# Kernel optimization log

Hardware: AMD Instinct MI355X
Metric: run time of the kernel (lower is better)

The kernel has to match this reference:

```python
import jax, jax.numpy as jnp
import numpy as np

N, E, G, F = 50000, 800000, 128, 64  # nodes, edges, graphs, feature dim
EPS = 1e-5


def setup_inputs() -> dict:
    key = jax.random.key(0)
    ks = jax.random.split(key, 16)
    w = lambda k, s: jax.random.normal(k, s, jnp.float32) * 0.05
    inp = {
        "x": jax.random.normal(ks[0], (N, F), jnp.float32),
        # SAGEConv l: lin_l (aggregated neighbors, with bias), lin_r (root, no bias)
        "c0_Wl": w(ks[1], (F, F)), "c0_bl": jnp.zeros((F,), jnp.float32), "c0_Wr": w(ks[2], (F, F)),
        "c1_Wl": w(ks[3], (F, F)), "c1_bl": jnp.zeros((F,), jnp.float32), "c1_Wr": w(ks[4], (F, F)),
        "c2_Wl": w(ks[5], (F, F)), "c2_bl": jnp.zeros((F,), jnp.float32), "c2_Wr": w(ks[6], (F, F)),
        # skip linears (bias=False)
        "s0_W": w(ks[7], (F, F)), "s1_W": w(ks[8], (F, F)),
        # graph-mode LayerNorm affine params
        "ln0_w": jnp.ones((F,), jnp.float32), "ln0_b": jnp.zeros((F,), jnp.float32),
        "ln1_w": jnp.ones((F,), jnp.float32), "ln1_b": jnp.zeros((F,), jnp.float32),
        "ln2_w": jnp.ones((F,), jnp.float32), "ln2_b": jnp.zeros((F,), jnp.float32),
        # PReLU(1): single shared slope, torch default init 0.25
        "p0_a": jnp.full((1,), 0.25, jnp.float32),
        "p1_a": jnp.full((1,), 0.25, jnp.float32),
        "p2_a": jnp.full((1,), 0.25, jnp.float32),
        "edge_index": jax.random.randint(ks[9], (2, E), 0, N, jnp.int64),
        "batch": jnp.sort(jax.random.randint(ks[10], (N,), 0, G, jnp.int64)),
    }
    return inp


def _sage(x, Wl, bl, Wr, src, dst):
    # mean-aggregate source features at destinations, then two linears
    agg = jax.ops.segment_sum(x[src], dst, num_segments=N)            # [N, F]
    deg = jax.ops.segment_sum(jnp.ones((E,), x.dtype), dst, num_segments=N)
    agg = agg / jnp.maximum(deg, 1.0)[:, None]
    return agg @ Wl + bl + x @ Wr


def _graph_ln(x, batch, w, b):
    # PyG LayerNorm mode='graph': normalize over all nodes & channels per graph
    f = x.shape[-1]
    cnt = jax.ops.segment_sum(jnp.ones((x.shape[0],), x.dtype), batch, num_segments=G)
    norm = jnp.maximum(cnt, 1.0) * f                                  # [G]
    mean = jax.ops.segment_sum(x, batch, num_segments=G).sum(-1) / norm
    xc = x - mean[batch][:, None]
    var = jax.ops.segment_sum(xc * xc, batch, num_segments=G).sum(-1) / norm
    out = xc / jnp.sqrt(var + EPS)[batch][:, None]
    return out * w + b


def _prelu(x, a):
    return jnp.where(x >= 0, x, a[0] * x)


def reference(x, c0_Wl, c0_bl, c0_Wr, c1_Wl, c1_bl, c1_Wr, c2_Wl, c2_bl, c2_Wr,
              s0_W, s1_W, ln0_w, ln0_b, ln1_w, ln1_b, ln2_w, ln2_b,
              p0_a, p1_a, p2_a, edge_index, batch):
    src, dst = edge_index[0], edge_index[1]
    h1 = _prelu(_graph_ln(_sage(x, c0_Wl, c0_bl, c0_Wr, src, dst), batch, ln0_w, ln0_b), p0_a)
    h2 = _sage(h1 + x @ s0_W, c1_Wl, c1_bl, c1_Wr, src, dst)
    h2 = _prelu(_graph_ln(h2, batch, ln1_w, ln1_b), p1_a)
    ret = _sage(h1 + h2 + x @ s1_W, c2_Wl, c2_bl, c2_Wr, src, dst)
    ret = _prelu(_graph_ln(ret, batch, ln2_w, ln2_b), p2_a)
    return ret
```

## Files before the change

kernel.cpp:

```cpp
#include <hip/hip_runtime.h>

#define NN 50000
#define NE 800000
#define NG 128
#define NF 64
#define EPSV 1e-5f
#define GB3 782
#define NBUCK 196
#define BCAP 5120

typedef unsigned short ushortT;

__device__ inline unsigned short f2bf(float f) {
  unsigned u = __float_as_uint(f);
  u += 0x7FFF + ((u >> 16) & 1);
  return (unsigned short)(u >> 16);
}

__global__ void k_bz(const int* __restrict__ batch, int* __restrict__ bound,
                     int* __restrict__ gcursor, float* __restrict__ stats) {
  int i = blockIdx.x * 256 + threadIdx.x;
  if (blockIdx.x == 0) {
    int t = threadIdx.x;
    if (t < NBUCK) gcursor[t] = 0;
    for (int k = t; k < 6 * NG; k += 256) stats[k] = 0.f;
  }
  if (i >= NN) return;
  int b1 = batch[i];
  int b0 = (i == 0) ? -1 : batch[i - 1];
  for (int g = b0 + 1; g <= b1; ++g) bound[g] = i;
  if (i == NN - 1) {
    for (int g = b1 + 1; g <= NG; ++g) bound[g] = NN;
  }
}

__global__ __launch_bounds__(256) void k_cvt(const float* __restrict__ in,
                                             ushortT* __restrict__ outb) {
  int t = blockIdx.x * 256 + threadIdx.x;
  if (t >= NN * NF / 4) return;
  float4 v = ((const float4*)in)[t];
  ushortT4_t: ;
  ushort4 o;
  o.x = f2bf(v.x); o.y = f2bf(v.y); o.z = f2bf(v.z); o.w = f2bf(v.w);
  ((ushort4*)outb)[t] = o;
}

__global__ __launch_bounds__(256) void k_binA(const int* __restrict__ src,
                                              const int* __restrict__ dst,
                                              int* __restrict__ gcursor,
                                              int2* __restrict__ bbuf) {
  __shared__ int cnt[NBUCK], base[NBUCK], rank[NBUCK];
  int tid = threadIdx.x;
  if (tid < NBUCK) { cnt[tid] = 0; rank[tid] = 0; }
  __syncthreads();
  int e0 = blockIdx.x * 4096;
  int sv[16], dv[16], bk[16];
#pragma unroll
  for (int i = 0; i < 16; ++i) {
    int e = e0 + i * 256 + tid;
    if (e < NE) {
      sv[i] = src[e];
      dv[i] = dst[e];
      bk[i] = dv[i] >> 8;
      atomicAdd(&cnt[bk[i]], 1);
    } else bk[i] = -1;
  }
  __syncthreads();
  if (tid < NBUCK && cnt[tid] > 0) base[tid] = atomicAdd(&gcursor[tid], cnt[tid]);
  __syncthreads();
#pragma unroll
  for (int i = 0; i < 16; ++i) {
    if (bk[i] >= 0) {
      int p = base[bk[i]] + atomicAdd(&rank[bk[i]], 1);
      if (p < BCAP) bbuf[(size_t)bk[i] * BCAP + p] = make_int2(sv[i], dv[i]);
    }
  }
}

__global__ __launch_bounds__(256) void k_bscan(const int* __restrict__ gcursor,
                                               int* __restrict__ bbase,
                                               int* __restrict__ off) {
  __shared__ int sh[256];
  int tid = threadIdx.x;
  int v = (tid < NBUCK) ? gcursor[tid] : 0;
  sh[tid] = v;
  __syncthreads();
  for (int d = 1; d < 256; d <<= 1) {
    int t = (tid >= d) ? sh[tid - d] : 0;
    __syncthreads();
    sh[tid] += t;
    __syncthreads();
  }
  if (tid < NBUCK) bbase[tid] = sh[tid] - v;
  if (tid == NBUCK - 1) { bbase[NBUCK] = sh[tid]; off[NN] = sh[tid]; }
}

__global__ __launch_bounds__(256) void k_binB(const int2* __restrict__ bbuf,
                                              const int* __restrict__ gcursor,
                                              const int* __restrict__ bbase,
                                              int* __restrict__ off,
                                              int* __restrict__ csr) {
  __shared__ int cnt[256], cur[256], sh[256];
  int tid = threadIdx.x;
  int b = blockIdx.x;
  int nb = gcursor[b]; if (nb > BCAP) nb = BCAP;
  int gbase = bbase[b];
  cnt[tid] = 0;
  __syncthreads();
  const int2* bp = bbuf + (size_t)b * BCAP;
  for (int i = tid; i < nb; i += 256) {
    atomicAdd(&cnt[bp[i].y & 255], 1);
  }
  __syncthreads();
  int v = cnt[tid];
  sh[tid] = v;
  __syncthreads();
  for (int d = 1; d < 256; d <<= 1) {
    int t = (tid >= d) ? sh[tid - d] : 0;
    __syncthreads();
    sh[tid] += t;
    __syncthreads();
  }
  int excl = sh[tid] - v;
  cur[tid] = excl;
  int node = b * 256 + tid;
  if (node < NN) off[node] = gbase + excl;
  __syncthreads();
  for (int i = tid; i < nb; i += 256) {
    int2 e = bp[i];
    int p = atomicAdd(&cur[e.y & 255], 1);
    csr[gbase + p] = e.x;
  }
}

__global__ __launch_bounds__(256) void k_agg(const ushortT* __restrict__ in,
                                             const int* __restrict__ off,
                                             const int* __restrict__ csr,
                                             float* __restrict__ out) {
  int t = blockIdx.x * 256 + threadIdx.x;
  int node = t >> 6;
  int lane = threadIdx.x & 63;
  int eo = lane >> 3;
  int fl = (lane & 7) << 3;
  if (node >= NN) return;
  int s0 = off[node], s1 = off[node + 1];
  float a0 = 0.f, a1 = 0.f, a2 = 0.f, a3 = 0.f, a4 = 0.f, a5 = 0.f, a6 = 0.f, a7 = 0.f;
  for (int j = s0 + eo; j < s1; j += 8) {
    int s = csr[j];
    uint4 v = *(const uint4*)&in[(size_t)s * NF + fl];
    a0 += __uint_as_float(v.x << 16);
    a1 += __uint_as_float(v.x & 0xFFFF0000u);
    a2 += __uint_as_float(v.y << 16);
    a3 += __uint_as_float(v.y & 0xFFFF0000u);
    a4 += __uint_as_float(v.z << 16);
    a5 += __uint_as_float(v.z & 0xFFFF0000u);
    a6 += __uint_as_float(v.w << 16);
    a7 += __uint_as_float(v.w & 0xFFFF0000u);
  }
#pragma unroll
  for (int d = 8; d < 64; d <<= 1) {
    a0 += __shfl_xor(a0, d); a1 += __shfl_xor(a1, d);
    a2 += __shfl_xor(a2, d); a3 += __shfl_xor(a3, d);
    a4 += __shfl_xor(a4, d); a5 += __shfl_xor(a5, d);
    a6 += __shfl_xor(a6, d); a7 += __shfl_xor(a7, d);
  }
  if (eo == 0) {
    int dg = s1 - s0;
    float inv = (dg > 0) ? 1.f / (float)dg : 0.f;
    float4* op = (float4*)&out[(size_t)node * NF + fl];
    op[0] = make_float4(a0 * inv, a1 * inv, a2 * inv, a3 * inv);
    op[1] = make_float4(a4 * inv, a5 * inv, a6 * inv, a7 * inv);
  }
}

__global__ __launch_bounds__(256) void k_sage_linear(const float* __restrict__ A,
                                                     const float* __restrict__ X,
                                                     const float* __restrict__ Wl,
                                                     const float* __restrict__ bl,
                                                     const float* __restrict__ Wr,
                                                     const int* __restrict__ batch,
                                                     float* __restrict__ gsum,
                                                     float* __restrict__ gsq,
                                                     float* __restrict__ out) {
  __shared__ float sh_s[4][64];
  __shared__ float sh_q[4][64];
  __shared__ float gs[NG];
  __shared__ float gq[NG];
  int tid = threadIdx.x;
  int lane = tid & 63;
  int wv = __builtin_amdgcn_readfirstlane(tid >> 6);
  int c0 = wv * 16;
  int row = blockIdx.x * 64 + lane;
  bool valid = row < NN;
  if (tid < NG) { gs[tid] = 0.f; gq[tid] = 0.f; }

  float acc[16];
#pragma unroll
  for (int cc = 0; cc < 16; ++cc) acc[cc] = bl[c0 + cc];

  int rsafe = valid ? row : 0;
  const float4* Ar = (const float4*)(A + (size_t)rsafe * NF);
  const float4* Xr = (const float4*)(X + (size_t)rsafe * NF);

  for (int k4 = 0; k4 < 16; ++k4) {
    float4 av = Ar[k4];
    const float* W0 = Wl + ((k4 * 4 + 0) * NF + c0);
    const float* W1 = Wl + ((k4 * 4 + 1) * NF + c0);
    const float* W2 = Wl + ((k4 * 4 + 2) * NF + c0);
    const float* W3 = Wl + ((k4 * 4 + 3) * NF + c0);
#pragma unroll
    for (int cc = 0; cc < 16; ++cc)
      acc[cc] += av.x * W0[cc] + av.y * W1[cc] + av.z * W2[cc] + av.w * W3[cc];
  }
  for (int k4 = 0; k4 < 16; ++k4) {
    float4 xv = Xr[k4];
    const float* W0 = Wr + ((k4 * 4 + 0) * NF + c0);
    const float* W1 = Wr + ((k4 * 4 + 1) * NF + c0);
    const float* W2 = Wr + ((k4 * 4 + 2) * NF + c0);
    const float* W3 = Wr + ((k4 * 4 + 3) * NF + c0);
#pragma unroll
    for (int cc = 0; cc < 16; ++cc)
      acc[cc] += xv.x * W0[cc] + xv.y * W1[cc] + xv.z * W2[cc] + xv.w * W3[cc];
  }

  if (valid) {
    float4* op = (float4*)(out + (size_t)row * NF + c0);
    op[0] = make_float4(acc[0], acc[1], acc[2], acc[3]);
    op[1] = make_float4(acc[4], acc[5], acc[6], acc[7]);
    op[2] = make_float4(acc[8], acc[9], acc[10], acc[11]);
    op[3] = make_float4(acc[12], acc[13], acc[14], acc[15]);
  }

  float s = 0.f, q = 0.f;
#pragma unroll
  for (int cc = 0; cc < 16; ++cc) { s += acc[cc]; q += acc[cc] * acc[cc]; }
  sh_s[wv][lane] = s;
  sh_q[wv][lane] = q;
  __syncthreads();
  if (tid < 64) {
    float ss = sh_s[0][lane] + sh_s[1][lane] + sh_s[2][lane] + sh_s[3][lane];
    float qq = sh_q[0][lane] + sh_q[1][lane] + sh_q[2][lane] + sh_q[3][lane];
    int r = blockIdx.x * 64 + lane;
    if (r < NN) {
      int g = batch[r];
      atomicAdd(&gs[g], ss);
      atomicAdd(&gq[g], qq);
    }
  }
  __syncthreads();
  if (tid < NG) {
    float fs = gs[tid], fq = gq[tid];
    if (fs != 0.f || fq != 0.f) { atomicAdd(&gsum[tid], fs); atomicAdd(&gsq[tid], fq); }
  }
}

__global__ __launch_bounds__(256) void k_skip_linear(
    const float* __restrict__ X, const float* __restrict__ W,
    const float* __restrict__ t0, const float* __restrict__ gsum0, const float* __restrict__ gsq0,
    const float* __restrict__ lw0, const float* __restrict__ lb0, const float* __restrict__ pa0,
    const float* __restrict__ t1, const float* __restrict__ gsum1, const float* __restrict__ gsq1,
    const float* __restrict__ lw1, const float* __restrict__ lb1, const float* __restrict__ pa1,
    const int* __restrict__ batch, const int* __restrict__ bound,
    float* __restrict__ out, ushortT* __restrict__ outb) {
  int tid = threadIdx.x;
  int lane = tid & 63;
  int wv = __builtin_amdgcn_readfirstlane(tid >> 6);
  int c0 = wv * 16;
  int row = blockIdx.x * 64 + lane;
  bool valid = row < NN;
  int rsafe = valid ? row : 0;

  float acc[16];
#pragma unroll
  for (int cc = 0; cc < 16; ++cc) acc[cc] = 0.f;

  const float4* Xr = (const float4*)(X + (size_t)rsafe * NF);
  for (int k4 = 0; k4 < 16; ++k4) {
    float4 xv = Xr[k4];
    const float* W0 = W + ((k4 * 4 + 0) * NF + c0);
    const float* W1 = W + ((k4 * 4 + 1) * NF + c0);
    const float* W2 = W + ((k4 * 4 + 2) * NF + c0);
    const float* W3 = W + ((k4 * 4 + 3) * NF + c0);
#pragma unroll
    for (int cc = 0; cc < 16; ++cc)
      acc[cc] += xv.x * W0[cc] + xv.y * W1[cc] + xv.z * W2[cc] + xv.w * W3[cc];
  }

  int g = batch[rsafe];
  float cntf = (float)(bound[g + 1] - bound[g]);
  float norm = fmaxf(cntf, 1.f) * (float)NF;
  {
    float m0 = gsum0[g] / norm;
    float v0 = gsq0[g] / norm - m0 * m0;
    float rs0 = rsqrtf(v0 + EPSV);
    float a0 = pa0[0];
    const float4* T0 = (const float4*)(t0 + (size_t)rsafe * NF + c0);
#pragma unroll
    for (int j = 0; j < 4; ++j) {
      float4 tv = T0[j];
      float tvv[4] = {tv.x, tv.y, tv.z, tv.w};
#pragma unroll
      for (int jj = 0; jj < 4; ++jj) {
        int cc = j * 4 + jj;
        float u = (tvv[jj] - m0) * rs0 * lw0[c0 + cc] + lb0[c0 + cc];
        acc[cc] += (u >= 0.f) ? u : a0 * u;
      }
    }
  }
  if (t1) {
    float m1 = gsum1[g] / norm;
    float v1 = gsq1[g] / norm - m1 * m1;
    float rs1 = rsqrtf(v1 + EPSV);
    float a1 = pa1[0];
    const float4* T1 = (const float4*)(t1 + (size_t)rsafe * NF + c0);
#pragma unroll
    for (int j = 0; j < 4; ++j) {
      float4 tv = T1[j];
      float tvv[4] = {tv.x, tv.y, tv.z, tv.w};
#pragma unroll
      for (int jj = 0; jj < 4; ++jj) {
        int cc = j * 4 + jj;
        float u = (tvv[jj] - m1) * rs1 * lw1[c0 + cc] + lb1[c0 + cc];
        acc[cc] += (u >= 0.f) ? u : a1 * u;
      }
    }
  }

  if (valid) {
    float4* op = (float4*)(out + (size_t)row * NF + c0);
    op[0] = make_float4(acc[0], acc[1], acc[2], acc[3]);
    op[1] = make_float4(acc[4], acc[5], acc[6], acc[7]);
    op[2] = make_float4(acc[8], acc[9], acc[10], acc[11]);
    op[3] = make_float4(acc[12], acc[13], acc[14], acc[15]);
    uint4 b0, b1v;
    b0.x = (unsigned)f2bf(acc[0]) | ((unsigned)f2bf(acc[1]) << 16);
    b0.y = (unsigned)f2bf(acc[2]) | ((unsigned)f2bf(acc[3]) << 16);
    b0.z = (unsigned)f2bf(acc[4]) | ((unsigned)f2bf(acc[5]) << 16);
    b0.w = (unsigned)f2bf(acc[6]) | ((unsigned)f2bf(acc[7]) << 16);
    b1v.x = (unsigned)f2bf(acc[8]) | ((unsigned)f2bf(acc[9]) << 16);
    b1v.y = (unsigned)f2bf(acc[10]) | ((unsigned)f2bf(acc[11]) << 16);
    b1v.z = (unsigned)f2bf(acc[12]) | ((unsigned)f2bf(acc[13]) << 16);
    b1v.w = (unsigned)f2bf(acc[14]) | ((unsigned)f2bf(acc[15]) << 16);
    uint4* obp = (uint4*)&outb[(size_t)row * NF + c0];
    obp[0] = b0;
    obp[1] = b1v;
  }
}

__global__ __launch_bounds__(256) void k_ln_apply(const float* __restrict__ t,
                                                  const int* __restrict__ batch,
                                                  const int* __restrict__ bound,
                                                  const float* __restrict__ gsum,
                                                  const float* __restrict__ gsq,
                                                  const float* __restrict__ w,
                                                  const float* __restrict__ b,
                                                  const float* __restrict__ alpha,
                                                  float* __restrict__ out) {
  int wid = (blockIdx.x * 256 + threadIdx.x) >> 6;
  int lane = threadIdx.x & 63;
  if (wid >= NN) return;
  int g = batch[wid];
  float cnt = (float)(bound[g + 1] - bound[g]);
  float norm = fmaxf(cnt, 1.f) * (float)NF;
  float mean = gsum[g] / norm;
  float var = gsq[g] / norm - mean * mean;
  float rstd = rsqrtf(var + EPSV);
  float a = alpha[0];
  float v = t[wid * NF + lane];
  v = (v - mean) * rstd;
  v = v * w[lane] + b[lane];
  out[wid * NF + lane] = (v >= 0.f) ? v : a * v;
}

extern "C" void kernel_launch(void* const* d_in, const int* in_sizes, int n_in,
                              void* d_out, int out_size, void* d_ws, size_t ws_size,
                              hipStream_t stream) {
  const float* x     = (const float*)d_in[0];
  const float* c0_Wl = (const float*)d_in[1];
  const float* c0_bl = (const float*)d_in[2];
  const float* c0_Wr = (const float*)d_in[3];
  const float* c1_Wl = (const float*)d_in[4];
  const float* c1_bl = (const float*)d_in[5];
  const float* c1_Wr = (const float*)d_in[6];
  const float* c2_Wl = (const float*)d_in[7];
  const float* c2_bl = (const float*)d_in[8];
  const float* c2_Wr = (const float*)d_in[9];
  const float* s0_W  = (const float*)d_in[10];
  const float* s1_W  = (const float*)d_in[11];
  const float* ln0_w = (const float*)d_in[12];
  const float* ln0_b = (const float*)d_in[13];
  const float* ln1_w = (const float*)d_in[14];
  const float* ln1_b = (const float*)d_in[15];
  const float* ln2_w = (const float*)d_in[16];
  const float* ln2_b = (const float*)d_in[17];
  const float* p0_a  = (const float*)d_in[18];
  const float* p1_a  = (const float*)d_in[19];
  const float* p2_a  = (const float*)d_in[20];
  const int*   ei    = (const int*)d_in[21];
  const int*   batch = (const int*)d_in[22];
  float* out = (float*)d_out;

  const int* src = ei;
  const int* dst = ei + NE;

  char* ws = (char*)d_ws;
  const size_t off_gcur   = 0;
  const size_t off_stats  = 200704;
  const size_t off_bound  = 204800;
  const size_t off_off    = 205824;
  const size_t off_bbase  = 406272;
  const size_t off_csr    = 607744;
  const size_t off_B1     = 3807744;
  const size_t off_B2     = off_B1 + 12800000;
  const size_t off_B3     = off_B2 + 12800000;
  const size_t off_B4     = off_B3 + 12800000;
  const size_t off_xb     = off_B4 + 12800000;
  const size_t off_B3b    = off_xb + 6400000;

  int*    gcursor = (int*)(ws + off_gcur);
  float*  stats   = (float*)(ws + off_stats);
  int*    bound   = (int*)(ws + off_bound);
  int*    offp    = (int*)(ws + off_off);
  int*    bbase   = (int*)(ws + off_bbase);
  int*    csr     = (int*)(ws + off_csr);
  float*  B1      = (float*)(ws + off_B1);
  int2*   bbuf    = (int2*)(ws + off_B1);
  float*  B2      = (float*)(ws + off_B2);
  float*  B3      = (float*)(ws + off_B3);
  float*  B4      = (float*)(ws + off_B4);
  ushortT* xb     = (ushortT*)(ws + off_xb);
  ushortT* B3b    = (ushortT*)(ws + off_B3b);
  (void)ws_size; (void)in_sizes; (void)n_in; (void)out_size;

  float* gsum0 = stats + 0 * NG; float* gsq0 = stats + 1 * NG;
  float* gsum1 = stats + 2 * NG; float* gsq1 = stats + 3 * NG;
  float* gsum2 = stats + 4 * NG; float* gsq2 = stats + 5 * NG;

  const int NB  = (NN + 255) / 256;
  const int WB  = (NN * 64 + 255) / 256;
  const int CB  = (NN * NF / 4 + 255) / 256;

  k_bz<<<NB, 256, 0, stream>>>(batch, bound, gcursor, stats);
  k_cvt<<<CB, 256, 0, stream>>>(x, xb);
  k_binA<<<NBUCK, 256, 0, stream>>>(src, dst, gcursor, bbuf);
  k_bscan<<<1, 256, 0, stream>>>(gcursor, bbase, offp);
  k_binB<<<NBUCK, 256, 0, stream>>>(bbuf, gcursor, bbase, offp, csr);

  k_agg<<<WB, 256, 0, stream>>>(xb, offp, csr, B1);
  k_sage_linear<<<GB3, 256, 0, stream>>>(B1, x, c0_Wl, c0_bl, c0_Wr, batch, gsum0, gsq0, B2);
  k_skip_linear<<<GB3, 256, 0, stream>>>(x, s0_W,
                                         B2, gsum0, gsq0, ln0_w, ln0_b, p0_a,
                                         nullptr, nullptr, nullptr, nullptr, nullptr, nullptr,
                                         batch, bound, B3, B3b);

  k_agg<<<WB, 256, 0, stream>>>(B3b, offp, csr, B1);
  k_sage_linear<<<GB3, 256, 0, stream>>>(B1, B3, c1_Wl, c1_bl, c1_Wr, batch, gsum1, gsq1, B4);
  k_skip_linear<<<GB3, 256, 0, stream>>>(x, s1_W,
                                         B2, gsum0, gsq0, ln0_w, ln0_b, p0_a,
                                         B4, gsum1, gsq1, ln1_w, ln1_b, p1_a,
                                         batch, bound, B3, B3b);

  k_agg<<<WB, 256, 0, stream>>>(B3b, offp, csr, B1);
  k_sage_linear<<<GB3, 256, 0, stream>>>(B1, B3, c2_Wl, c2_bl, c2_Wr, batch, gsum2, gsq2, out);
  k_ln_apply<<<WB, 256, 0, stream>>>(out, batch, bound, gsum2, gsq2, ln2_w, ln2_b, p2_a, out);
}
```

Measured before the change: 223.5 us.

## Fuse neighbor mean aggregation into SAGE linear kernel via shared memory

Replaces the separate aggregation and linear kernels with one kernel per layer. Each block gathers bf16 neighbor features for its 64 nodes into LDS, stages the root features in LDS, then runs the two 64x64 linears plus the LayerNorm statistic accumulation. This removes the intermediate aggregated-feature buffer round trip through global memory and one launch per layer. The gather now runs with far fewer waves, each processing 16 nodes sequentially, which may reduce latency hiding for the irregular gather.

```diff
diff --git a/kernel.cpp b/kernel.cpp
--- a/kernel.cpp
+++ b/kernel.cpp
@@ -8,6 +8,7 @@
 #define GB3 782
 #define NBUCK 196
 #define BCAP 5120
+#define LDP 68
 
 typedef unsigned short ushortT;
 
@@ -39,7 +40,6 @@
   int t = blockIdx.x * 256 + threadIdx.x;
   if (t >= NN * NF / 4) return;
   float4 v = ((const float4*)in)[t];
-  ushortT4_t: ;
   ushort4 o;
   o.x = f2bf(v.x); o.y = f2bf(v.y); o.z = f2bf(v.z); o.w = f2bf(v.w);
   ((ushort4*)outb)[t] = o;
@@ -133,55 +133,19 @@
   }
 }
 
-__global__ __launch_bounds__(256) void k_agg(const ushortT* __restrict__ in,
-                                             const int* __restrict__ off,
-                                             const int* __restrict__ csr,
-                                             float* __restrict__ out) {
-  int t = blockIdx.x * 256 + threadIdx.x;
-  int node = t >> 6;
-  int lane = threadIdx.x & 63;
-  int eo = lane >> 3;
-  int fl = (lane & 7) << 3;
-  if (node >= NN) return;
-  int s0 = off[node], s1 = off[node + 1];
-  float a0 = 0.f, a1 = 0.f, a2 = 0.f, a3 = 0.f, a4 = 0.f, a5 = 0.f, a6 = 0.f, a7 = 0.f;
-  for (int j = s0 + eo; j < s1; j += 8) {
-    int s = csr[j];
-    uint4 v = *(const uint4*)&in[(size_t)s * NF + fl];
-    a0 += __uint_as_float(v.x << 16);
-    a1 += __uint_as_float(v.x & 0xFFFF0000u);
-    a2 += __uint_as_float(v.y << 16);
-    a3 += __uint_as_float(v.y & 0xFFFF0000u);
-    a4 += __uint_as_float(v.z << 16);
-    a5 += __uint_as_float(v.z & 0xFFFF0000u);
-    a6 += __uint_as_float(v.w << 16);
-    a7 += __uint_as_float(v.w & 0xFFFF0000u);
-  }
-#pragma unroll
-  for (int d = 8; d < 64; d <<= 1) {
-    a0 += __shfl_xor(a0, d); a1 += __shfl_xor(a1, d);
-    a2 += __shfl_xor(a2, d); a3 += __shfl_xor(a3, d);
-    a4 += __shfl_xor(a4, d); a5 += __shfl_xor(a5, d);
-    a6 += __shfl_xor(a6, d); a7 += __shfl_xor(a7, d);
-  }
-  if (eo == 0) {
-    int dg = s1 - s0;
-    float inv = (dg > 0) ? 1.f / (float)dg : 0.f;
-    float4* op = (float4*)&out[(size_t)node * NF + fl];
-    op[0] = make_float4(a0 * inv, a1 * inv, a2 * inv, a3 * inv);
-    op[1] = make_float4(a4 * inv, a5 * inv, a6 * inv, a7 * inv);
-  }
-}
-
-__global__ __launch_bounds__(256) void k_sage_linear(const float* __restrict__ A,
-                                                     const float* __restrict__ X,
-                                                     const float* __restrict__ Wl,
-                                                     const float* __restrict__ bl,
-                                                     const float* __restrict__ Wr,
-                                                     const int* __restrict__ batch,
-                                                     float* __restrict__ gsum,
-                                                     float* __restrict__ gsq,
-                                                     float* __restrict__ out) {
+__global__ __launch_bounds__(256) void k_sage_fused(const ushortT* __restrict__ inb,
+                                                    const int* __restrict__ off,
+                                                    const int* __restrict__ csr,
+                                                    const float* __restrict__ X,
+                                                    const float* __restrict__ Wl,
+                                                    const float* __restrict__ bl,
+                                                    const float* __restrict__ Wr,
+                                                    const int* __restrict__ batch,
+                                                    float* __restrict__ gsum,
+                                                    float* __restrict__ gsq,
+                                                    float* __restrict__ out) {
+  __shared__ float sA[64][LDP];
+  __shared__ float sX[64][LDP];
   __shared__ float sh_s[4][64];
   __shared__ float sh_q[4][64];
   __shared__ float gs[NG];
@@ -189,21 +153,65 @@
   int tid = threadIdx.x;
   int lane = tid & 63;
   int wv = __builtin_amdgcn_readfirstlane(tid >> 6);
+  int nodebase = blockIdx.x * 64;
+  if (tid < NG) { gs[tid] = 0.f; gq[tid] = 0.f; }
+
+#pragma unroll
+  for (int q = 0; q < 4; ++q) {
+    int r = q * 16 + (tid >> 4);
+    int c4 = tid & 15;
+    int gr = nodebase + r;
+    int rs = (gr < NN) ? gr : 0;
+    float4 v = *(const float4*)&X[(size_t)rs * NF + c4 * 4];
+    *(float4*)&sX[r][c4 * 4] = v;
+  }
+
+  int eo = lane >> 3;
+  int fl = (lane & 7) << 3;
+  for (int i = 0; i < 16; ++i) {
+    int node = nodebase + wv * 16 + i;
+    if (node >= NN) break;
+    int s0 = off[node], s1 = off[node + 1];
+    float a0 = 0.f, a1 = 0.f, a2 = 0.f, a3 = 0.f, a4 = 0.f, a5 = 0.f, a6 = 0.f, a7 = 0.f;
+    for (int j = s0 + eo; j < s1; j += 8) {
+      int s = csr[j];
+      uint4 v = *(const uint4*)&inb[(size_t)s * NF + fl];
+      a0 += __uint_as_float(v.x << 16);
+      a1 += __uint_as_float(v.x & 0xFFFF0000u);
+      a2 += __uint_as_float(v.y << 16);
+      a3 += __uint_as_float(v.y & 0xFFFF0000u);
+      a4 += __uint_as_float(v.z << 16);
+      a5 += __uint_as_float(v.z & 0xFFFF0000u);
+      a6 += __uint_as_float(v.w << 16);
+      a7 += __uint_as_float(v.w & 0xFFFF0000u);
+    }
+#pragma unroll
+    for (int d = 8; d < 64; d <<= 1) {
+      a0 += __shfl_xor(a0, d); a1 += __shfl_xor(a1, d);
+      a2 += __shfl_xor(a2, d); a3 += __shfl_xor(a3, d);
+      a4 += __shfl_xor(a4, d); a5 += __shfl_xor(a5, d);
+      a6 += __shfl_xor(a6, d); a7 += __shfl_xor(a7, d);
+    }
+    if (eo == 0) {
+      int dg = s1 - s0;
+      float inv = (dg > 0) ? 1.f / (float)dg : 0.f;
+      int rl = wv * 16 + i;
+      *(float4*)&sA[rl][fl]     = make_float4(a0 * inv, a1 * inv, a2 * inv, a3 * inv);
+      *(float4*)&sA[rl][fl + 4] = make_float4(a4 * inv, a5 * inv, a6 * inv, a7 * inv);
+    }
+  }
+  __syncthreads();
+
   int c0 = wv * 16;
-  int row = blockIdx.x * 64 + lane;
+  int row = nodebase + lane;
   bool valid = row < NN;
-  if (tid < NG) { gs[tid] = 0.f; gq[tid] = 0.f; }
 
   float acc[16];
 #pragma unroll
   for (int cc = 0; cc < 16; ++cc) acc[cc] = bl[c0 + cc];
 
-  int rsafe = valid ? row : 0;
-  const float4* Ar = (const float4*)(A + (size_t)rsafe * NF);
-  const float4* Xr = (const float4*)(X + (size_t)rsafe * NF);
-
   for (int k4 = 0; k4 < 16; ++k4) {
-    float4 av = Ar[k4];
+    float4 av = *(const float4*)&sA[lane][k4 * 4];
     const float* W0 = Wl + ((k4 * 4 + 0) * NF + c0);
     const float* W1 = Wl + ((k4 * 4 + 1) * NF + c0);
     const float* W2 = Wl + ((k4 * 4 + 2) * NF + c0);
@@ -213,7 +221,7 @@
       acc[cc] += av.x * W0[cc] + av.y * W1[cc] + av.z * W2[cc] + av.w * W3[cc];
   }
   for (int k4 = 0; k4 < 16; ++k4) {
-    float4 xv = Xr[k4];
+    float4 xv = *(const float4*)&sX[lane][k4 * 4];
     const float* W0 = Wr + ((k4 * 4 + 0) * NF + c0);
     const float* W1 = Wr + ((k4 * 4 + 1) * NF + c0);
     const float* W2 = Wr + ((k4 * 4 + 2) * NF + c0);
@@ -240,7 +248,7 @@
   if (tid < 64) {
     float ss = sh_s[0][lane] + sh_s[1][lane] + sh_s[2][lane] + sh_s[3][lane];
     float qq = sh_q[0][lane] + sh_q[1][lane] + sh_q[2][lane] + sh_q[3][lane];
-    int r = blockIdx.x * 64 + lane;
+    int r = nodebase + lane;
     if (r < NN) {
       int g = batch[r];
       atomicAdd(&gs[g], ss);
@@ -423,7 +431,6 @@
   int*    offp    = (int*)(ws + off_off);
   int*    bbase   = (int*)(ws + off_bbase);
   int*    csr     = (int*)(ws + off_csr);
-  float*  B1      = (float*)(ws + off_B1);
   int2*   bbuf    = (int2*)(ws + off_B1);
   float*  B2      = (float*)(ws + off_B2);
   float*  B3      = (float*)(ws + off_B3);
@@ -446,21 +453,21 @@
   k_bscan<<<1, 256, 0, stream>>>(gcursor, bbase, offp);
   k_binB<<<NBUCK, 256, 0, stream>>>(bbuf, gcursor, bbase, offp, csr);
 
-  k_agg<<<WB, 256, 0, stream>>>(xb, offp, csr, B1);
-  k_sage_linear<<<GB3, 256, 0, stream>>>(B1, x, c0_Wl, c0_bl, c0_Wr, batch, gsum0, gsq0, B2);
+  k_sage_fused<<<GB3, 256, 0, stream>>>(xb, offp, csr, x, c0_Wl, c0_bl, c0_Wr,
+                                        batch, gsum0, gsq0, B2);
   k_skip_linear<<<GB3, 256, 0, stream>>>(x, s0_W,
                                          B2, gsum0, gsq0, ln0_w, ln0_b, p0_a,
                                          nullptr, nullptr, nullptr, nullptr, nullptr, nullptr,
                                          batch, bound, B3, B3b);
 
-  k_agg<<<WB, 256, 0, stream>>>(B3b, offp, csr, B1);
-  k_sage_linear<<<GB3, 256, 0, stream>>>(B1, B3, c1_Wl, c1_bl, c1_Wr, batch, gsum1, gsq1, B4);
+  k_sage_fused<<<GB3, 256, 0, stream>>>(B3b, offp, csr, B3, c1_Wl, c1_bl, c1_Wr,
+                                        batch, gsum1, gsq1, B4);
   k_skip_linear<<<GB3, 256, 0, stream>>>(x, s1_W,
                                          B2, gsum0, gsq0, ln0_w, ln0_b, p0_a,
                                          B4, gsum1, gsq1, ln1_w, ln1_b, p1_a,
                                          batch, bound, B3, B3b);
 
-  k_agg<<<WB, 256, 0, stream>>>(B3b, offp, csr, B1);
-  k_sage_linear<<<GB3, 256, 0, stream>>>(B1, B3, c2_Wl, c2_bl, c2_Wr, batch, gsum2, gsq2, out);
+  k_sage_fused<<<GB3, 256, 0, stream>>>(B3b, offp, csr, B3, c2_Wl, c2_bl, c2_Wr,
+                                        batch, gsum2, gsq2, out);
   k_ln_apply<<<WB, 256, 0, stream>>>(out, batch, bound, gsum2, gsq2, ln2_w, ln2_b, p2_a, out);
 }
```

Measured after the change: 245.3 us. 1.1x slower.
